# Kernel optimization log

Measured on AMD Instinct MI355X. Metric: run time of the kernel, lower is better.

The kernel has to match this reference:

```python
import jax, jax.numpy as jnp
import numpy as np

SEQ, N = 8192, 1024
W_SYN = 20.0

# ArcTan surrogate spike fn ('ArcTan', alpha=1.0, beta=10.0): forward = Heaviside
@jax.custom_vjp
def spike(x):
    return (x > 0).astype(x.dtype)

def _spike_fwd(x):
    return spike(x), x

def _spike_bwd(x, g):
    return (g * (1.0 / (1.0 + (10.0 * x) ** 2)),)

spike.defvjp(_spike_fwd, _spike_bwd)


def setup_inputs() -> dict:
    key = jax.random.key(0)
    k_in, = jax.random.split(key, 1)
    input_batch = jax.random.normal(k_in, (SEQ, N), dtype=jnp.float32)
    state = jnp.zeros((2, N), jnp.float32)  # (v, u)
    # learned params, sized per init_kwargs
    W1 = jnp.eye(N, dtype=jnp.float32) * W_SYN          # f1.ff.weight [N, N]
    W2 = jnp.ones((1, N), jnp.float32) * W_SYN          # f2.ff.weight [1, N]
    a = jnp.full((N,), 0.02, jnp.float32)
    b = jnp.full((N,), 0.2, jnp.float32)
    c = jnp.full((N,), -65.0, jnp.float32)
    d = jnp.full((N,), 8.0, jnp.float32)
    thresh = jnp.full((N,), 30.0, jnp.float32)
    dt = jnp.full((N,), 1.0, jnp.float32)               # time_step per neuron
    leak = jnp.full((1,), 0.99, jnp.float32)            # decode leak
    return dict(input_batch=input_batch, state=state, W1=W1, W2=W2,
                a=a, b=b, c=c, d=d, thresh=thresh, dt=dt, leak=leak)


def reference(input_batch, state, W1, W2, a, b, c, d, thresh, dt, leak):
    v0, u0 = state[0], state[1]
    dm0 = jnp.zeros((1,), input_batch.dtype)  # decode_mempot starts at 0

    def step(carry, x_t):
        v, u, dm = carry
        I = W1 @ x_t  # synaptic current [N]
        # Izhikevich ODE (Euler step)
        v_new = v + dt * (0.04 * v * v + 5.0 * v + 140.0 - u + I)
        u_new = u + dt * a * (b * v - u)
        s = spike(v_new - thresh)
        v_out = v_new * (1.0 - s) + c * s   # reset v -> c on spike
        u_out = u_new + d * s               # u -> u + d on spike
        dm_new = leak * dm + W2 @ s         # leaky-integrator decode [1]
        return (v_out, u_out, dm_new), (s, jnp.stack([v_out, u_out]), dm_new)

    _, (outputs, states, decoded) = jax.lax.scan(step, (v0, u0, dm0), input_batch)
    return outputs, states, decoded  # [T,N], [T,2,N], [T,1]
```

## Files before the change

### kernel.cpp

```cpp
#include <hip/hip_runtime.h>

#define CAP 32
#define K 16

__global__ void sparsify_kernel(const float* __restrict__ W1, int N,
                                int* __restrict__ cnts, int* __restrict__ cols,
                                float* __restrict__ wts) {
  __shared__ int scnt;
  const int row = blockIdx.x;
  if (threadIdx.x == 0) scnt = 0;
  __syncthreads();
  const float* wr = W1 + (long)row * N;
  for (int k = threadIdx.x; k < N; k += blockDim.x) {
    float w = wr[k];
    if (w != 0.0f) {
      int slot = atomicAdd(&scnt, 1);
      if (slot < CAP) {
        cols[row * CAP + slot] = k;
        wts[row * CAP + slot] = w;
      }
    }
  }
  __syncthreads();
  if (threadIdx.x == 0) {
    cnts[row] = scnt;
    if (scnt == 0) { cols[row * CAP] = 0; wts[row * CAP] = 0.0f; }
  }
}

__global__ void touch_kernel(const float4* __restrict__ x4, long n4,
                             float* __restrict__ dump) {
  long i = (long)blockIdx.x * blockDim.x + threadIdx.x;
  const long stride = (long)gridDim.x * blockDim.x;
  float acc = 0.f;
  for (; i < n4; i += stride) {
    float4 v = x4[i];
    acc += v.x + v.y + v.z + v.w;
  }
  if (acc == 1234.56789f) dump[blockIdx.x & 1023] = acc;
}

#define IZH_STEP(xv, sout)                        \
  {                                               \
    const float I = w0 * (xv);                    \
    float t1 = 0.04f * v;                         \
    float t2 = t1 * v;                            \
    float t3 = 5.0f * v;                          \
    float t4 = t2 + t3;                           \
    float t5 = t4 + 140.0f;                       \
    float t6 = t5 - u;                            \
    float t7 = t6 + I;                            \
    float vn = v + t7;          \
    float q1 = bn * v;                            \
    float q2 = q1 - u;                            \
    float q3 = Pn * q2;                           \
    float un = u + q3;                            \
    float df = vn - thn;                          \
    bool sp = df > 0.0f;                          \
    v = sp ? cn : vn;        \
    u = un + (sp ? dn : 0.0f);   \
    sout = sp ? 1.0f : 0.0f;                      \
  }

__global__ void __launch_bounds__(256) izh_pipe_kernel(
    const float* __restrict__ X, const float* __restrict__ state,
    const float* __restrict__ a, const float* __restrict__ b,
    const float* __restrict__ c, const float* __restrict__ d,
    const float* __restrict__ th, const float* __restrict__ dtv,
    const float* __restrict__ W1,
    const int* __restrict__ cnts, const int* __restrict__ cols,
    const float* __restrict__ wts,
    float* __restrict__ o_s, float* __restrict__ o_st,
    int T, int N)
{
#pragma clang fp contract(off)
  __shared__ float xbuf[2][K][64];
  __shared__ float obuf[2][K][3][64];
  __shared__ int s_fast;

  const int wid  = threadIdx.x >> 6;
  const int lane = threadIdx.x & 63;
  const int base = blockIdx.x * 64;
  const int gn   = base + lane;
  const int B    = T / K;
  const long N2  = 2L * N;

  if (wid == 0) {
    bool elig = (base + 64 <= N) && ((N & 3) == 0);
    if (elig) elig = (cnts[gn] == 1) && (dtv[gn] == 1.0f);
    unsigned long long m = __ballot(elig);
    if (lane == 0) s_fast = (m == ~0ULL) ? 1 : 0;
  }
  __syncthreads();

  if (s_fast) {
    float v = 0.f, u = 0.f, an = 0.f, bn = 0.f, cn = 0.f, dn = 0.f;
    float thn = 0.f, Pn = 0.f, w0 = 0.f;
    int c0g = 0;
    float xreg[K];
    int c0l = 0;

    if (wid == 0) {
      v = state[gn]; u = state[N + gn];
      an = a[gn]; bn = b[gn]; cn = c[gn]; dn = d[gn]; thn = th[gn];
      Pn = dtv[gn] * an;
      w0 = wts[gn * CAP];
      c0g = cols[gn * CAP];
    } else if (wid == 1) {
      c0l = cols[gn * CAP];
      if (B >= 1) {
        float r0[K];
#pragma unroll
        for (int i = 0; i < K; ++i) r0[i] = X[(size_t)i * N + c0l];
#pragma unroll
        for (int i = 0; i < K; ++i) xbuf[0][i][lane] = r0[i];
      }
      if (B >= 2) {
#pragma unroll
        for (int i = 0; i < K; ++i) xreg[i] = X[(size_t)(K + i) * N + c0l];
      }
    }
    __syncthreads();

    auto store4 = [&](float* P, long RS, int q, int cidx) {
      const int r = lane >> 4, j = lane & 15;
      const int t0 = q * K;
#pragma unroll
      for (int i = 0; i < K; i += 4) {
        const int t = t0 + i + r;
        float4 val = *(const float4*)&obuf[q & 1][i + r][cidx][4 * j];
        *(float4*)(P + (size_t)t * RS + base + 4 * j) = val;
      }
    };

    for (int k = 0; k < B; ++k) {
      if (wid == 0) {
        float xv[K];
#pragma unroll
        for (int i = 0; i < K; ++i) xv[i] = xbuf[k & 1][i][lane];
#pragma unroll
        for (int i = 0; i < K; ++i) {
          float s_;
          IZH_STEP(xv[i], s_);
          obuf[k & 1][i][0][lane] = s_;
          obuf[k & 1][i][1][lane] = v;
          obuf[k & 1][i][2][lane] = u;
        }
      } else if (wid == 1) {
        if (k + 1 < B) {
#pragma unroll
          for (int i = 0; i < K; ++i) xbuf[(k + 1) & 1][i][lane] = xreg[i];
        }
        if (k + 2 < B) {
#pragma unroll
          for (int i = 0; i < K; ++i)
            xreg[i] = X[(size_t)((k + 2) * K + i) * N + c0l];
        }
        if (k > 0) store4(o_s, N, k - 1, 0);
      } else if (wid == 2) {
        if (k > 0) store4(o_st, N2, k - 1, 1);
      } else {
        if (k > 0) store4(o_st + N, N2, k - 1, 2);
      }
      __syncthreads();
    }

    if (B > 0) {
      if (wid == 1)      store4(o_s, N, B - 1, 0);
      else if (wid == 2) store4(o_st, N2, B - 1, 1);
      else if (wid == 3) store4(o_st + N, N2, B - 1, 2);
    }

    if (wid == 0) {
      const float* xp = X + c0g;
      for (int t = B * K; t < T; ++t) {
        const float xv = xp[(size_t)t * N];
        float s_;
        IZH_STEP(xv, s_);
        o_s[(size_t)t * N + gn] = s_;
        o_st[(size_t)t * N2 + gn] = v;
        o_st[(size_t)t * N2 + N + gn] = u;
      }
    }
  } else {
    if (wid != 0 || gn >= N) return;
    float v = state[gn], u = state[N + gn];
    const float an = a[gn], bn = b[gn], cn = c[gn], dn = d[gn];
    const float thn = th[gn], dtn = dtv[gn];
    const float Pn = dtn * an;
    const int cnt = cnts[gn];
    for (int t = 0; t < T; ++t) {
      float I = 0.0f;
      if (cnt <= CAP) {
        for (int j = 0; j < cnt; ++j)
          I = I + wts[gn * CAP + j] * X[(size_t)t * N + cols[gn * CAP + j]];
      } else {
        const float* wr = W1 + (size_t)gn * N;
        const float* xr = X + (size_t)t * N;
        for (int kk = 0; kk < N; ++kk) I = I + wr[kk] * xr[kk];
      }
      float t1 = 0.04f * v; float t2 = t1 * v; float t3 = 5.0f * v;
      float t4 = t2 + t3; float t5 = t4 + 140.0f; float t6 = t5 - u;
      float t7 = t6 + I; float t8 = dtn * t7; float vn = v + t8;
      float q1 = bn * v; float q2 = q1 - u; float q3 = Pn * q2; float un = u + q3;
      float df = vn - thn; bool sp = df > 0.0f;
      v = sp ? cn : vn; u = un + (sp ? dn : 0.0f);
      o_s[(size_t)t * N + gn] = sp ? 1.0f : 0.0f;
      o_st[(size_t)t * N2 + gn] = v;
      o_st[(size_t)t * N2 + N + gn] = u;
    }
  }
}

__global__ void decode_dot_kernel(const float* __restrict__ o_s,
                                  const float* __restrict__ W2,
                                  float* __restrict__ r, int N) {
  const int t = blockIdx.x;
  const float* srow = o_s + (long)t * N;
  float p = 0.0f;
  for (int n = threadIdx.x; n < N; n += blockDim.x)
    p += W2[n] * srow[n];
  for (int off = 32; off > 0; off >>= 1) p += __shfl_down(p, off);
  __shared__ float red[4];
  if ((threadIdx.x & 63) == 0) red[threadIdx.x >> 6] = p;
  __syncthreads();
  if (threadIdx.x == 0) {
    float tot = 0.f;
    const int nw = blockDim.x >> 6;
    for (int w = 0; w < nw; ++w) tot += red[w];
    r[t] = tot;
  }
}

__global__ void decode_scan_kernel(const float* __restrict__ r,
                                   const float* __restrict__ leakp,
                                   float* __restrict__ out, int T) {
  __shared__ float Bsh[64], Ssh[64];
  const float leakv = leakp[0];
  const int i = threadIdx.x;
  const int chunk = (T + 63) / 64;
  const int t0 = i * chunk;
  float B = 0.0f;
  for (int j = 0; j < chunk; ++j) {
    int t = t0 + j;
    if (t < T) B = leakv * B + r[t];
  }
  Bsh[i] = B;
  float A = 1.0f, p = leakv; int e = chunk;
  while (e) { if (e & 1) A *= p; p *= p; e >>= 1; }
  __syncthreads();
  if (i == 0) {
    float dm = 0.0f;
    for (int k = 0; k < 64; ++k) { Ssh[k] = dm; dm = A * dm + Bsh[k]; }
  }
  __syncthreads();
  float dm = Ssh[i];
  for (int j = 0; j < chunk; ++j) {
    int t = t0 + j;
    if (t < T) { dm = leakv * dm + r[t]; out[t] = dm; }
  }
}

extern "C" void kernel_launch(void* const* d_in, const int* in_sizes, int n_in,
                              void* d_out, int out_size, void* d_ws, size_t ws_size,
                              hipStream_t stream) {
  const float* X  = (const float*)d_in[0];
  const float* st = (const float*)d_in[1];
  const float* W1 = (const float*)d_in[2];
  const float* W2 = (const float*)d_in[3];
  const float* a  = (const float*)d_in[4];
  const float* b  = (const float*)d_in[5];
  const float* c  = (const float*)d_in[6];
  const float* d  = (const float*)d_in[7];
  const float* th = (const float*)d_in[8];
  const float* dt = (const float*)d_in[9];
  const float* lk = (const float*)d_in[10];
  const int N = in_sizes[4];
  const int T = in_sizes[0] / N;

  float* o_s  = (float*)d_out;
  float* o_st = o_s + (long)T * N;
  float* o_dm = o_st + 2L * (long)T * N;

  int*   cnts = (int*)d_ws;
  int*   cols = cnts + N;
  float* wts  = (float*)(cols + (long)N * CAP);
  float* rbuf = wts + (long)N * CAP;
  float* dump = rbuf + T;

  sparsify_kernel<<<N, 256, 0, stream>>>(W1, N, cnts, cols, wts);
  const long n4 = ((long)T * N) / 4;
  touch_kernel<<<1024, 256, 0, stream>>>((const float4*)X, n4, dump);
  const int nblk = (N + 63) / 64;
  izh_pipe_kernel<<<nblk, 256, 0, stream>>>(X, st, a, b, c, d, th, dt, W1,
                                            cnts, cols, wts, o_s, o_st, T, N);
  decode_dot_kernel<<<T, 256, 0, stream>>>(o_s, W2, rbuf, N);
  decode_scan_kernel<<<1, 64, 0, stream>>>(rbuf, lk, o_dm, T);
}
```

Before: 592.5 us.

## Replace warp-specialized LDS pipeline with single-wave register double-buffered kernel

The four-wave producer/consumer kernel, which staged X through shared memory and used separate waves to store outputs, becomes a single 64-thread wave per block. That wave prefetches X into two register arrays (ping-pong) and writes outputs directly to global memory, with the batch size raised to 32. This removes the per-batch __syncthreads and the shared-memory round trips. In exchange, the direct stores are no longer float4-vectorized, more registers are used, and the serial recurrence wave now issues all stores itself.

```diff
diff --git a/kernel.cpp b/kernel.cpp
--- a/kernel.cpp
+++ b/kernel.cpp
@@ -1,7 +1,7 @@
 #include <hip/hip_runtime.h>
 
 #define CAP 32
-#define K 16
+#define K 32
 
 __global__ void sparsify_kernel(const float* __restrict__ W1, int N,
                                 int* __restrict__ cnts, int* __restrict__ cols,
@@ -62,7 +62,7 @@
     sout = sp ? 1.0f : 0.0f;                      \
   }
 
-__global__ void __launch_bounds__(256) izh_pipe_kernel(
+__global__ void __launch_bounds__(64) izh_wave_kernel(
     const float* __restrict__ X, const float* __restrict__ state,
     const float* __restrict__ a, const float* __restrict__ b,
     const float* __restrict__ c, const float* __restrict__ d,
@@ -74,116 +74,71 @@
     int T, int N)
 {
 #pragma clang fp contract(off)
-  __shared__ float xbuf[2][K][64];
-  __shared__ float obuf[2][K][3][64];
-  __shared__ int s_fast;
-
-  const int wid  = threadIdx.x >> 6;
   const int lane = threadIdx.x & 63;
   const int base = blockIdx.x * 64;
   const int gn   = base + lane;
-  const int B    = T / K;
   const long N2  = 2L * N;
 
-  if (wid == 0) {
-    bool elig = (base + 64 <= N) && ((N & 3) == 0);
-    if (elig) elig = (cnts[gn] == 1) && (dtv[gn] == 1.0f);
-    unsigned long long m = __ballot(elig);
-    if (lane == 0) s_fast = (m == ~0ULL) ? 1 : 0;
-  }
-  __syncthreads();
-
-  if (s_fast) {
-    float v = 0.f, u = 0.f, an = 0.f, bn = 0.f, cn = 0.f, dn = 0.f;
-    float thn = 0.f, Pn = 0.f, w0 = 0.f;
-    int c0g = 0;
-    float xreg[K];
-    int c0l = 0;
-
-    if (wid == 0) {
-      v = state[gn]; u = state[N + gn];
-      an = a[gn]; bn = b[gn]; cn = c[gn]; dn = d[gn]; thn = th[gn];
-      Pn = dtv[gn] * an;
-      w0 = wts[gn * CAP];
-      c0g = cols[gn * CAP];
-    } else if (wid == 1) {
-      c0l = cols[gn * CAP];
-      if (B >= 1) {
-        float r0[K];
+  bool elig = (base + 64 <= N);
+  if (elig) elig = (cnts[gn] == 1) && (dtv[gn] == 1.0f);
+  const bool fast = (__ballot(elig) == ~0ULL);
+
+  if (fast) {
+    float v = state[gn], u = state[N + gn];
+    const float an  = a[gn], bn = b[gn], cn = c[gn], dn = d[gn];
+    const float thn = th[gn];
+    const float Pn  = dtv[gn] * an;
+    const float w0  = wts[gn * CAP];
+    const int   c0  = cols[gn * CAP];
+    const int   B   = T / K;
+    const float* Xp = X + c0;
+
+    float xA[K], xB[K];
+    if (B >= 1) {
 #pragma unroll
-        for (int i = 0; i < K; ++i) r0[i] = X[(size_t)i * N + c0l];
+      for (int i = 0; i < K; ++i) xA[i] = Xp[(size_t)i * N];
+    }
+
+#define DO_BATCH(XR, kk)                                   \
+    {                                                      \
+      long tS = (long)(kk) * K * N;                        \
+      long tV = (long)(kk) * K * N2;                       \
+      _Pragma("unroll")                                    \
+      for (int i = 0; i < K; ++i) {                        \
+        float s_;                                          \
+        IZH_STEP(XR[i], s_);                               \
+        o_s[tS + gn] = s_;                                 \
+        o_st[tV + gn] = v;                                 \
+        o_st[tV + N + gn] = u;                             \
+        tS += N; tV += N2;                                 \
+      }                                                    \
+    }
+
+    int k = 0;
+    for (; k + 1 < B; k += 2) {
 #pragma unroll
-        for (int i = 0; i < K; ++i) xbuf[0][i][lane] = r0[i];
+      for (int i = 0; i < K; ++i)
+        xB[i] = Xp[(size_t)((k + 1) * K + i) * N];
+      DO_BATCH(xA, k);
+      if (k + 2 < B) {
+#pragma unroll
+        for (int i = 0; i < K; ++i)
+          xA[i] = Xp[(size_t)((k + 2) * K + i) * N];
       }
-      if (B >= 2) {
-#pragma unroll
-        for (int i = 0; i < K; ++i) xreg[i] = X[(size_t)(K + i) * N + c0l];
-      }
-    }
-    __syncthreads();
-
-    auto store4 = [&](float* P, long RS, int q, int cidx) {
-      const int r = lane >> 4, j = lane & 15;
-      const int t0 = q * K;
-#pragma unroll
-      for (int i = 0; i < K; i += 4) {
-        const int t = t0 + i + r;
-        float4 val = *(const float4*)&obuf[q & 1][i + r][cidx][4 * j];
-        *(float4*)(P + (size_t)t * RS + base + 4 * j) = val;
-      }
-    };
-
-    for (int k = 0; k < B; ++k) {
-      if (wid == 0) {
-        float xv[K];
-#pragma unroll
-        for (int i = 0; i < K; ++i) xv[i] = xbuf[k & 1][i][lane];
-#pragma unroll
-        for (int i = 0; i < K; ++i) {
-          float s_;
-          IZH_STEP(xv[i], s_);
-          obuf[k & 1][i][0][lane] = s_;
-          obuf[k & 1][i][1][lane] = v;
-          obuf[k & 1][i][2][lane] = u;
-        }
-      } else if (wid == 1) {
-        if (k + 1 < B) {
-#pragma unroll
-          for (int i = 0; i < K; ++i) xbuf[(k + 1) & 1][i][lane] = xreg[i];
-        }
-        if (k + 2 < B) {
-#pragma unroll
-          for (int i = 0; i < K; ++i)
-            xreg[i] = X[(size_t)((k + 2) * K + i) * N + c0l];
-        }
-        if (k > 0) store4(o_s, N, k - 1, 0);
-      } else if (wid == 2) {
-        if (k > 0) store4(o_st, N2, k - 1, 1);
-      } else {
-        if (k > 0) store4(o_st + N, N2, k - 1, 2);
-      }
-      __syncthreads();
-    }
-
-    if (B > 0) {
-      if (wid == 1)      store4(o_s, N, B - 1, 0);
-      else if (wid == 2) store4(o_st, N2, B - 1, 1);
-      else if (wid == 3) store4(o_st + N, N2, B - 1, 2);
-    }
-
-    if (wid == 0) {
-      const float* xp = X + c0g;
-      for (int t = B * K; t < T; ++t) {
-        const float xv = xp[(size_t)t * N];
-        float s_;
-        IZH_STEP(xv, s_);
-        o_s[(size_t)t * N + gn] = s_;
-        o_st[(size_t)t * N2 + gn] = v;
-        o_st[(size_t)t * N2 + N + gn] = u;
-      }
-    }
+      DO_BATCH(xB, k + 1);
+    }
+    if (k < B) DO_BATCH(xA, k);
+
+    for (int t = B * K; t < T; ++t) {
+      float s_;
+      IZH_STEP(Xp[(size_t)t * N], s_);
+      o_s[(long)t * N + gn] = s_;
+      o_st[(long)t * N2 + gn] = v;
+      o_st[(long)t * N2 + N + gn] = u;
+    }
+#undef DO_BATCH
   } else {
-    if (wid != 0 || gn >= N) return;
+    if (gn >= N) return;
     float v = state[gn], u = state[N + gn];
     const float an = a[gn], bn = b[gn], cn = c[gn], dn = d[gn];
     const float thn = th[gn], dtn = dtv[gn];
@@ -292,8 +247,8 @@
   const long n4 = ((long)T * N) / 4;
   touch_kernel<<<1024, 256, 0, stream>>>((const float4*)X, n4, dump);
   const int nblk = (N + 63) / 64;
-  izh_pipe_kernel<<<nblk, 256, 0, stream>>>(X, st, a, b, c, d, th, dt, W1,
-                                            cnts, cols, wts, o_s, o_st, T, N);
+  izh_wave_kernel<<<nblk, 64, 0, stream>>>(X, st, a, b, c, d, th, dt, W1,
+                                           cnts, cols, wts, o_s, o_st, T, N);
   decode_dot_kernel<<<T, 256, 0, stream>>>(o_s, W2, rbuf, N);
   decode_scan_kernel<<<1, 64, 0, stream>>>(rbuf, lk, o_dm, T);
 }
```

After: 791.2 us. +33.5%, slower.
